# Kernel optimization log

Measured on AMD Instinct MI355X. Metric: run time of the kernel, lower is better.

The kernel has to match this reference:

```python
import jax, jax.numpy as jnp
import numpy as np

N_NODES = 50000
N_EDGES = 1600000
HID = 128
N_LAYERS = 4
EPS = 1e-5
NEG_SLOPE = 0.2


def setup_inputs() -> dict:
    key = jax.random.key(0)
    ks = jax.random.split(key, 10)
    x = jax.random.normal(ks[0], (N_NODES, HID), dtype=jnp.float32)
    edge_index = jax.random.randint(ks[1], (2, N_EDGES), 0, N_NODES, dtype=jnp.int64)
    edge_label_index = jax.random.randint(ks[2], (2, 8192), 0, N_NODES, dtype=jnp.int64)
    s = 1.0 / np.sqrt(HID)
    Wl = jax.random.uniform(ks[3], (N_LAYERS, HID, HID), jnp.float32, -s, s)
    Wr = jax.random.uniform(ks[4], (N_LAYERS, HID, HID), jnp.float32, -s, s)
    att = jax.random.uniform(ks[5], (N_LAYERS, HID), jnp.float32, -s, s)
    bias = jnp.zeros((N_LAYERS, HID), jnp.float32)
    gamma = jnp.ones((N_LAYERS, HID), jnp.float32)
    beta = jnp.zeros((N_LAYERS, HID), jnp.float32)
    return {"x": x, "edge_index": edge_index, "edge_label_index": edge_label_index,
            "Wl": Wl, "Wr": Wr, "att": att, "bias": bias, "gamma": gamma, "beta": beta}


def _gatv2_layer(x, Wl, Wr, a, b, src, dst):
    # GATv2Conv, single head: e_ij = a^T LeakyReLU(W_l x_j + W_r x_i)
    xl = x @ Wl                       # [N, H] source transform (also the message)
    xr = x @ Wr                       # [N, H] target transform
    e = jax.nn.leaky_relu(xl[src] + xr[dst], NEG_SLOPE) @ a   # [E]
    emax = jax.ops.segment_max(e, dst, num_segments=N_NODES)  # per-target max
    ew = jnp.exp(e - emax[dst])
    denom = jax.ops.segment_sum(ew, dst, num_segments=N_NODES)
    alpha = ew / denom[dst]
    out = jax.ops.segment_sum(alpha[:, None] * xl[src], dst, num_segments=N_NODES)
    return out + b


def _batchnorm(x, g, b):
    mu = jnp.mean(x, axis=0)
    var = jnp.mean(jnp.square(x - mu), axis=0)  # biased var (training mode)
    return (x - mu) * jax.lax.rsqrt(var + EPS) * g + b


def _embedding(x, edge_index, Wl, Wr, att, bias, gamma, beta):
    loops = jnp.arange(N_NODES, dtype=edge_index.dtype)
    src = jnp.concatenate([edge_index[0], loops])
    dst = jnp.concatenate([edge_index[1], loops])
    resw = 1.0 / (N_LAYERS + 1)  # alpha buffer, all entries equal
    h = x
    out = None
    for i in range(N_LAYERS):
        h = _gatv2_layer(h, Wl[i], Wr[i], att[i], bias[i], src, dst)
        h = _batchnorm(h, gamma[i], beta[i])
        out = h * resw if out is None else out + h * resw
    return out


def reference(x, edge_index, edge_label_index, Wl, Wr, att, bias, gamma, beta):
    out = _embedding(x, edge_index, Wl, Wr, att, bias, gamma, beta)
    return (out[edge_label_index[0]] * out[edge_label_index[1]]).sum(axis=-1)
```

## Files before the change

### kernel.cpp

```cpp
#include <hip/hip_runtime.h>
#include <hip/hip_bf16.h>
#include <hip/hip_fp16.h>

#define N_NODES 50000
#define N_EDGES 1600000
#define ET (N_EDGES + N_NODES)
#define HID 128
#define N_LAYERS 4
#define EPS 1e-5f
#define NEG 0.2f
#define RB 256
#define NBUCK 196
#define BCHUNK 8192
#define LOG2E 1.44269504088896f

typedef __attribute__((ext_vector_type(8))) short s16x8;
typedef __attribute__((ext_vector_type(8))) __bf16 bfx8;
typedef __attribute__((ext_vector_type(4))) float fx4;
typedef __attribute__((ext_vector_type(2))) _Float16 f16x2;

__device__ __forceinline__ unsigned int packbf2(float a, float b) {
    unsigned int ua = __float_as_uint(a);
    ua = (ua + 0x7fffu + ((ua >> 16) & 1u)) >> 16;
    unsigned int ub = __float_as_uint(b);
    ub = (ub + 0x7fffu + ((ub >> 16) & 1u)) & 0xffff0000u;
    return (ua & 0xffffu) | ub;
}
__device__ __forceinline__ unsigned short bf16r(float a) {
    unsigned int ua = __float_as_uint(a);
    return (unsigned short)((ua + 0x7fffu + ((ua >> 16) & 1u)) >> 16);
}
__device__ __forceinline__ unsigned int packh2(float a, float b) {
    return __builtin_bit_cast(unsigned int, __builtin_amdgcn_cvt_pkrtz(a, b));
}
__device__ __forceinline__ f16x2 packh2v(float a, float b) {
    return __builtin_bit_cast(f16x2, __builtin_amdgcn_cvt_pkrtz(a, b));
}
__device__ __forceinline__ float2 unpackh2(unsigned int u) {
    f16x2 h = __builtin_bit_cast(f16x2, u);
    return make_float2((float)h.x, (float)h.y);
}

__global__ void bucket_zero_kernel(int* __restrict__ gcnt, int* __restrict__ dhist) {
    int i = blockIdx.x * 256 + threadIdx.x;
    if (i < NBUCK) gcnt[i] = 0;
    if (i < 256) dhist[i] = 0;
}

__global__ __launch_bounds__(256) void bucket_hist_kernel(const int* __restrict__ ei,
                                                          int* __restrict__ gcnt) {
    __shared__ int h[NBUCK];
    for (int i = threadIdx.x; i < NBUCK; i += 256) h[i] = 0;
    __syncthreads();
    int base = blockIdx.x * BCHUNK;
    int lim = min(base + BCHUNK, ET);
    for (int i = base + threadIdx.x; i < lim; i += 256) {
        int dst = (i < N_EDGES) ? ei[N_EDGES + i] : i - N_EDGES;
        atomicAdd(&h[dst >> 8], 1);
    }
    __syncthreads();
    for (int i = threadIdx.x; i < NBUCK; i += 256)
        if (h[i]) atomicAdd(&gcnt[i], h[i]);
}

__global__ void bucket_scan_kernel(const int* __restrict__ gcnt, int* __restrict__ bbase,
                                   int* __restrict__ bcur, int* __restrict__ rowptr) {
    __shared__ int sh[256];
    int tid = threadIdx.x;
    int v = (tid < NBUCK) ? gcnt[tid] : 0;
    sh[tid] = v;
    __syncthreads();
    for (int off = 1; off < 256; off <<= 1) {
        int t = (tid >= off) ? sh[tid - off] : 0;
        __syncthreads();
        sh[tid] += t;
        __syncthreads();
    }
    if (tid < NBUCK) {
        int ex = sh[tid] - v;
        bbase[tid] = ex;
        bcur[tid] = ex;
    }
    if (tid == NBUCK - 1) bbase[NBUCK] = sh[tid];
    if (tid == 0) rowptr[N_NODES] = ET;
}

__global__ __launch_bounds__(256) void bucket_scatter_kernel(const int* __restrict__ ei,
                                                             int* __restrict__ bcur,
                                                             unsigned int* __restrict__ pairs) {
    __shared__ int h[NBUCK];
    __shared__ int rbase[NBUCK];
    for (int i = threadIdx.x; i < NBUCK; i += 256) h[i] = 0;
    __syncthreads();
    int base = blockIdx.x * BCHUNK;
    int lim = min(base + BCHUNK, ET);
    for (int i = base + threadIdx.x; i < lim; i += 256) {
        int dst = (i < N_EDGES) ? ei[N_EDGES + i] : i - N_EDGES;
        atomicAdd(&h[dst >> 8], 1);
    }
    __syncthreads();
    for (int i = threadIdx.x; i < NBUCK; i += 256) {
        rbase[i] = h[i] ? atomicAdd(&bcur[i], h[i]) : 0;
        h[i] = 0;
    }
    __syncthreads();
    for (int i = base + threadIdx.x; i < lim; i += 256) {
        int src, dst;
        if (i < N_EDGES) { src = ei[i]; dst = ei[N_EDGES + i]; }
        else { src = dst = i - N_EDGES; }
        int b = dst >> 8;
        int pos = rbase[b] + atomicAdd(&h[b], 1);
        pairs[pos] = (unsigned int)src | ((unsigned int)(dst & 255) << 16);
    }
}

__global__ __launch_bounds__(256) void bucket_sort_kernel(const unsigned int* __restrict__ pairs,
                                                          const int* __restrict__ bbase,
                                                          int* __restrict__ rowptr,
                                                          unsigned short* __restrict__ csr_src) {
    __shared__ int h[256], cur[256], sh[256];
    int b = blockIdx.x;
    int tid = threadIdx.x;
    h[tid] = 0;
    __syncthreads();
    int bs = bbase[b], be = bbase[b + 1];
    for (int i = bs + tid; i < be; i += 256) atomicAdd(&h[pairs[i] >> 16], 1);
    __syncthreads();
    int v = h[tid];
    sh[tid] = v;
    __syncthreads();
    for (int off = 1; off < 256; off <<= 1) {
        int u = (tid >= off) ? sh[tid - off] : 0;
        __syncthreads();
        sh[tid] += u;
        __syncthreads();
    }
    int ex = sh[tid] - v;
    cur[tid] = ex;
    int n0 = b * 256 + tid;
    if (n0 < N_NODES) rowptr[n0] = bs + ex;
    __syncthreads();
    for (int i = bs + tid; i < be; i += 256) {
        unsigned int u = pairs[i];
        int ln = u >> 16;
        int pos = bs + atomicAdd(&cur[ln], 1);
        csr_src[pos] = (unsigned short)(u & 0xffffu);
    }
}

__global__ __launch_bounds__(256) void deg_hist_kernel(const int* __restrict__ rowptr,
                                                       int* __restrict__ dhist) {
    __shared__ int h[256];
    h[threadIdx.x] = 0;
    __syncthreads();
    int n = blockIdx.x * 256 + threadIdx.x;
    if (n < N_NODES) {
        int cc = min((rowptr[n + 1] - rowptr[n] + 7) >> 3, 255);
        atomicAdd(&h[cc], 1);
    }
    __syncthreads();
    if (h[threadIdx.x]) atomicAdd(&dhist[threadIdx.x], h[threadIdx.x]);
}

__global__ void deg_scan_kernel(const int* __restrict__ dhist, int* __restrict__ dcur) {
    __shared__ int sh[256];
    int t = threadIdx.x;
    int v = dhist[t];
    sh[t] = v;
    __syncthreads();
    for (int off = 1; off < 256; off <<= 1) {
        int u = (t >= off) ? sh[t - off] : 0;
        __syncthreads();
        sh[t] += u;
        __syncthreads();
    }
    dcur[t] = sh[t] - v;
}

__global__ __launch_bounds__(256) void deg_scatter_kernel(const int* __restrict__ rowptr,
                                                          int* __restrict__ dcur,
                                                          int* __restrict__ perm) {
    __shared__ int h[256], rbase[256];
    int t = threadIdx.x;
    h[t] = 0;
    __syncthreads();
    int n = blockIdx.x * 256 + t;
    int cc = -1;
    if (n < N_NODES) {
        cc = min((rowptr[n + 1] - rowptr[n] + 7) >> 3, 255);
        atomicAdd(&h[cc], 1);
    }
    __syncthreads();
    rbase[t] = h[t] ? atomicAdd(&dcur[t], h[t]) : 0;
    h[t] = 0;
    __syncthreads();
    if (n < N_NODES) {
        int pos = rbase[cc] + atomicAdd(&h[cc], 1);
        perm[pos] = n;
    }
}

__global__ __launch_bounds__(256) void wconv_kernel(const float* __restrict__ Wl,
                                                    const float* __restrict__ Wr,
                                                    unsigned short* __restrict__ wt) {
    int m = blockIdx.x;
    const float* __restrict__ W = ((m & 1) ? Wr : Wl) + (size_t)(m >> 1) * HID * HID;
    unsigned short* __restrict__ o = wt + (size_t)m * HID * HID;
    for (int i = threadIdx.x; i < HID * HID; i += 256) {
        int k = i >> 7, c = i & 127;
        o[c * HID + k] = bf16r(W[i]);
    }
}

__global__ __launch_bounds__(256) void gemm_mfma_kernel(
    const float* __restrict__ hin_f, const unsigned int* __restrict__ hin_h,
    const unsigned short* __restrict__ wt_layer,
    unsigned int* __restrict__ xlh, unsigned int* __restrict__ xrh,
    const float* __restrict__ scale, const float* __restrict__ shift,
    unsigned int* __restrict__ accb, int donorm, int accmode) {
    __shared__ unsigned int Wsh[128 * 64];
    int row0 = blockIdx.x * 64;
    int tid = threadIdx.x;
    int w = tid >> 6, l = tid & 63;
    int lr = l & 15, lk = l >> 4;
    int node = row0 + w * 16 + lr;
    bool valid = node < N_NODES;

    bfx8 afrag[4];
#pragma unroll
    for (int kt = 0; kt < 4; kt++) {
        int ch = kt * 4 + lk;
        float4 va = make_float4(0.f, 0.f, 0.f, 0.f), vb = va;
        if (valid) {
            if (hin_h) {
                uint4 u = *(const uint4*)(hin_h + (size_t)node * 64 + ch * 4);
                float2 f0 = unpackh2(u.x), f1 = unpackh2(u.y);
                float2 f2 = unpackh2(u.z), f3 = unpackh2(u.w);
                va = make_float4(f0.x, f0.y, f1.x, f1.y);
                vb = make_float4(f2.x, f2.y, f3.x, f3.y);
            } else {
                const float4* src = (const float4*)(hin_f + (size_t)node * HID + ch * 8);
                va = src[0]; vb = src[1];
            }
            if (donorm) {
                const float4* s4 = (const float4*)(scale + ch * 8);
                const float4* t4 = (const float4*)(shift + ch * 8);
                float4 s0 = s4[0], s1 = s4[1], t0 = t4[0], t1 = t4[1];
                va.x = va.x * s0.x + t0.x; va.y = va.y * s0.y + t0.y;
                va.z = va.z * s0.z + t0.z; va.w = va.w * s0.w + t0.w;
                vb.x = vb.x * s1.x + t1.x; vb.y = vb.y * s1.y + t1.y;
                vb.z = vb.z * s1.z + t1.z; vb.w = vb.w * s1.w + t1.w;
            }
            if (accmode) {
                uint4* ap = (uint4*)(accb + (size_t)node * 64) + ch;
                uint4 av;
                if (accmode == 1) {
                    av.x = packh2(0.2f * va.x, 0.2f * va.y);
                    av.y = packh2(0.2f * va.z, 0.2f * va.w);
                    av.z = packh2(0.2f * vb.x, 0.2f * vb.y);
                    av.w = packh2(0.2f * vb.z, 0.2f * vb.w);
                } else {
                    uint4 old = *ap;
                    float2 o0 = unpackh2(old.x), o1 = unpackh2(old.y);
                    float2 o2 = unpackh2(old.z), o3 = unpackh2(old.w);
                    av.x = packh2(o0.x + 0.2f * va.x, o0.y + 0.2f * va.y);
                    av.y = packh2(o1.x + 0.2f * va.z, o1.y + 0.2f * va.w);
                    av.z = packh2(o2.x + 0.2f * vb.x, o2.y + 0.2f * vb.y);
                    av.w = packh2(o3.x + 0.2f * vb.z, o3.y + 0.2f * vb.w);
                }
                *ap = av;
            }
        }
        unsigned int pk0 = packbf2(va.x, va.y), pk1 = packbf2(va.z, va.w);
        unsigned int pk2 = packbf2(vb.x, vb.y), pk3 = packbf2(vb.z, vb.w);
        uint4 pk = make_uint4(pk0, pk1, pk2, pk3);
        afrag[kt] = __builtin_bit_cast(bfx8, pk);
    }

    for (int mat = 0; mat < 2; mat++) {
        if (mat) __syncthreads();
        const uint4* wm4 = (const uint4*)(wt_layer + (size_t)mat * HID * HID);
        for (int i = tid; i < 2048; i += 256) {
            int c = i >> 4, ch = i & 15;
            uint4 v = wm4[i];
            *(uint4*)(&Wsh[c * 64 + ((ch ^ (c & 7)) << 2)]) = v;
        }
        __syncthreads();

        fx4 acc[8];
#pragma unroll
        for (int ct = 0; ct < 8; ct++) acc[ct] = (fx4){0.f, 0.f, 0.f, 0.f};
#pragma unroll
        for (int kt = 0; kt < 4; kt++) {
            int ch = kt * 4 + lk;
#pragma unroll
            for (int ct = 0; ct < 8; ct++) {
                int c = ct * 16 + lr;
                bfx8 aw = __builtin_bit_cast(bfx8, *(const s16x8*)(&Wsh[c * 64 + ((ch ^ (c & 7)) << 2)]));
                acc[ct] = __builtin_amdgcn_mfma_f32_16x16x32_bf16(aw, afrag[kt], acc[ct], 0, 0, 0);
            }
        }
        unsigned int* o = mat ? xrh : xlh;
        if (valid) {
#pragma unroll
            for (int ct = 0; ct < 8; ct++) {
                int cb = ct * 8 + lk * 2;
                uint2 p0;
                p0.x = packh2(acc[ct][0], acc[ct][1]);
                p0.y = packh2(acc[ct][2], acc[ct][3]);
                *(uint2*)(o + (size_t)node * 64 + cb) = p0;
            }
        }
    }
}

__global__ __launch_bounds__(64) void aggregate_kernel(
    const unsigned int* __restrict__ xlh, const unsigned int* __restrict__ xrh,
    const float* __restrict__ att, const float* __restrict__ bias,
    const int* __restrict__ rowptr, const unsigned short* __restrict__ csr_src,
    const int* __restrict__ perm, unsigned int* __restrict__ hout) {
    int slot = blockIdx.x * 4 + (threadIdx.x >> 4);
    if (slot >= N_NODES) return;
    int node = perm[N_NODES - 1 - slot];
    int g = threadIdx.x & 15;
    int c0 = g * 8;
    float4 aa = *(const float4*)(att + c0);
    float4 ab = *(const float4*)(att + c0 + 4);
    f16x2 a0 = packh2v(aa.x * LOG2E, aa.y * LOG2E);
    f16x2 a1 = packh2v(aa.z * LOG2E, aa.w * LOG2E);
    f16x2 a2 = packh2v(ab.x * LOG2E, ab.y * LOG2E);
    f16x2 a3 = packh2v(ab.z * LOG2E, ab.w * LOG2E);
    const uint4 ru = *(const uint4*)(xrh + (size_t)node * 64 + g * 4);
    f16x2 r0 = __builtin_bit_cast(f16x2, ru.x), r1 = __builtin_bit_cast(f16x2, ru.y);
    f16x2 r2 = __builtin_bit_cast(f16x2, ru.z), r3 = __builtin_bit_cast(f16x2, ru.w);
    const f16x2 negc = {(_Float16)NEG, (_Float16)NEG};
    int beg = rowptr[node], end = rowptr[node + 1];
    bool b0 = (g & 1) != 0, b1 = (g & 2) != 0, b2 = (g & 4) != 0;
    int myj = g & 7;
    float spart = 0.f;
    float acc0 = 0.f, acc1 = 0.f, acc2 = 0.f, acc3 = 0.f;
    float acc4 = 0.f, acc5 = 0.f, acc6 = 0.f, acc7 = 0.f;
    int idxc = (int)csr_src[min(beg + myj, end - 1)];
    for (int base = beg; base < end; base += 8) {
        int nn = end - base;
        if (nn > 8) nn = 8;
        int idxn = (base + 8 < end) ? (int)csr_src[min(base + 8 + myj, end - 1)] : 0;
        uint4 v[8];
#pragma unroll
        for (int j = 0; j < 8; j++) {
            int sj = __shfl(idxc, j, 8);
            v[j] = *(const uint4*)(xlh + (size_t)sj * 64 + g * 4);
        }
        float p[8];
#pragma unroll
        for (int j = 0; j < 8; j++) {
            f16x2 v0 = __builtin_bit_cast(f16x2, v[j].x);
            f16x2 v1 = __builtin_bit_cast(f16x2, v[j].y);
            f16x2 v2 = __builtin_bit_cast(f16x2, v[j].z);
            f16x2 v3 = __builtin_bit_cast(f16x2, v[j].w);
            f16x2 s0 = v0 + r0, s1 = v1 + r1, s2 = v2 + r2, s3 = v3 + r3;
            f16x2 m0 = __builtin_elementwise_max(s0, s0 * negc);
            f16x2 m1 = __builtin_elementwise_max(s1, s1 * negc);
            f16x2 m2 = __builtin_elementwise_max(s2, s2 * negc);
            f16x2 m3 = __builtin_elementwise_max(s3, s3 * negc);
            p[j] = __builtin_amdgcn_fdot2(m0, a0,
                     __builtin_amdgcn_fdot2(m1, a1,
                       __builtin_amdgcn_fdot2(m2, a2,
                         __builtin_amdgcn_fdot2(m3, a3, 0.f, false), false), false), false);
        }
        float q0 = (b0 ? p[1] : p[0]) + __shfl_xor(b0 ? p[0] : p[1], 1);
        float q1 = (b0 ? p[3] : p[2]) + __shfl_xor(b0 ? p[2] : p[3], 1);
        float q2 = (b0 ? p[5] : p[4]) + __shfl_xor(b0 ? p[4] : p[5], 1);
        float q3 = (b0 ? p[7] : p[6]) + __shfl_xor(b0 ? p[6] : p[7], 1);
        float t0 = (b1 ? q1 : q0) + __shfl_xor(b1 ? q0 : q1, 2);
        float t1 = (b1 ? q3 : q2) + __shfl_xor(b1 ? q2 : q3, 2);
        float f  = (b2 ? t1 : t0) + __shfl_xor(b2 ? t0 : t1, 4);
        f += __shfl_xor(f, 8);
        float wown = (myj < nn) ? exp2f(f) : 0.f;
        spart += wown;
#pragma unroll
        for (int j = 0; j < 8; j++) {
            float wj = __shfl(wown, j, 8);
            f16x2 v0 = __builtin_bit_cast(f16x2, v[j].x);
            f16x2 v1 = __builtin_bit_cast(f16x2, v[j].y);
            f16x2 v2 = __builtin_bit_cast(f16x2, v[j].z);
            f16x2 v3 = __builtin_bit_cast(f16x2, v[j].w);
            acc0 += wj * (float)v0.x; acc1 += wj * (float)v0.y;
            acc2 += wj * (float)v1.x; acc3 += wj * (float)v1.y;
            acc4 += wj * (float)v2.x; acc5 += wj * (float)v2.y;
            acc6 += wj * (float)v3.x; acc7 += wj * (float)v3.y;
        }
        idxc = idxn;
    }
    float s = spart;
    s += __shfl_xor(s, 1);
    s += __shfl_xor(s, 2);
    s += __shfl_xor(s, 4);
    float inv = 1.f / s;
    float4 ba = *(const float4*)(bias + c0);
    float4 bb = *(const float4*)(bias + c0 + 4);
    uint4 po;
    po.x = packh2(acc0 * inv + ba.x, acc1 * inv + ba.y);
    po.y = packh2(acc2 * inv + ba.z, acc3 * inv + ba.w);
    po.z = packh2(acc4 * inv + bb.x, acc5 * inv + bb.y);
    po.w = packh2(acc6 * inv + bb.z, acc7 * inv + bb.w);
    *(uint4*)(hout + (size_t)node * 64 + g * 4) = po;
}

__global__ __launch_bounds__(256) void bn_reduce_kernel(const unsigned int* __restrict__ h,
                                                        float* __restrict__ part) {
    int tid = threadIdx.x;
    int cu = tid & 63, half = tid >> 6;
    float s0 = 0.f, q0 = 0.f, s1 = 0.f, q1 = 0.f;
    for (int r = blockIdx.x * 4 + half; r < N_NODES; r += RB * 4) {
        float2 v = unpackh2(h[(size_t)r * 64 + cu]);
        s0 += v.x; q0 += v.x * v.x;
        s1 += v.y; q1 += v.y * v.y;
    }
    __shared__ float sh[256];
    sh[half * 64 + cu] = s0;
    __syncthreads();
    if (tid < 64) {
        float r0 = sh[tid] + sh[64 + tid] + sh[128 + tid] + sh[192 + tid];
        part[blockIdx.x * 256 + tid * 2] = r0;
    }
    __syncthreads();
    sh[half * 64 + cu] = q0;
    __syncthreads();
    if (tid < 64) {
        float r0 = sh[tid] + sh[64 + tid] + sh[128 + tid] + sh[192 + tid];
        part[blockIdx.x * 256 + 128 + tid * 2] = r0;
    }
    __syncthreads();
    sh[half * 64 + cu] = s1;
    __syncthreads();
    if (tid < 64) {
        float r0 = sh[tid] + sh[64 + tid] + sh[128 + tid] + sh[192 + tid];
        part[blockIdx.x * 256 + tid * 2 + 1] = r0;
    }
    __syncthreads();
    sh[half * 64 + cu] = q1;
    __syncthreads();
    if (tid < 64) {
        float r0 = sh[tid] + sh[64 + tid] + sh[128 + tid] + sh[192 + tid];
        part[blockIdx.x * 256 + 128 + tid * 2 + 1] = r0;
    }
}

__global__ void bn_finalize_kernel(const float* __restrict__ part,
                                   const float* __restrict__ gamma,
                                   const float* __restrict__ beta,
                                   float* __restrict__ scale, float* __restrict__ shift) {
    int c = threadIdx.x;
    float s = 0.f, q = 0.f;
    for (int b = 0; b < RB; b++) {
        s += part[b * 256 + c];
        q += part[b * 256 + 128 + c];
    }
    float m = s / (float)N_NODES;
    float v = q / (float)N_NODES - m * m;
    if (v < 0.f) v = 0.f;
    float rs = rsqrtf(v + EPS);
    float sc = rs * gamma[c];
    scale[c] = sc;
    shift[c] = beta[c] - m * sc;
}

__global__ __launch_bounds__(256) void accb_kernel(const unsigned int* __restrict__ h,
                                                   const float* __restrict__ scale,
                                                   const float* __restrict__ shift,
                                                   unsigned int* __restrict__ acc) {
    int idx = blockIdx.x * 256 + threadIdx.x;
    if (idx >= N_NODES * 64) return;
    int c = (idx & 63) * 2;
    float2 v = unpackh2(h[idx]);
    float n0 = v.x * scale[c] + shift[c];
    float n1 = v.y * scale[c + 1] + shift[c + 1];
    float2 a = unpackh2(acc[idx]);
    acc[idx] = packh2(a.x + 0.2f * n0, a.y + 0.2f * n1);
}

__global__ __launch_bounds__(256) void predict_kernel(const unsigned int* __restrict__ acc,
                                                      const int* __restrict__ eli,
                                                      float* __restrict__ out) {
    int p = blockIdx.x * 4 + (threadIdx.x >> 6);
    if (p >= 8192) return;
    int lane = threadIdx.x & 63;
    int i = eli[p], j = eli[8192 + p];
    f16x2 va = __builtin_bit_cast(f16x2, acc[(size_t)i * 64 + lane]);
    f16x2 vb = __builtin_bit_cast(f16x2, acc[(size_t)j * 64 + lane]);
    float t = (float)va.x * (float)vb.x + (float)va.y * (float)vb.y;
#pragma unroll
    for (int off = 32; off; off >>= 1) t += __shfl_xor(t, off, 64);
    if (lane == 0) out[p] = t;
}

extern "C" void kernel_launch(void* const* d_in, const int* in_sizes, int n_in,
                              void* d_out, int out_size, void* d_ws, size_t ws_size,
                              hipStream_t stream) {
    const float* x = (const float*)d_in[0];
    const int* ei = (const int*)d_in[1];
    const int* eli = (const int*)d_in[2];
    const float* Wl = (const float*)d_in[3];
    const float* Wr = (const float*)d_in[4];
    const float* att = (const float*)d_in[5];
    const float* bias = (const float*)d_in[6];
    const float* gamma = (const float*)d_in[7];
    const float* beta = (const float*)d_in[8];
    float* out = (float*)d_out;

    char* ws = (char*)d_ws;
    size_t off = 0;
    unsigned int* hbuf = (unsigned int*)(ws + off); off += (size_t)N_NODES * HID * 2;
    unsigned int* accb = (unsigned int*)(ws + off); off += (size_t)N_NODES * HID * 2;
    unsigned int* xlh  = (unsigned int*)(ws + off); off += (size_t)N_NODES * HID * 2;
    unsigned int* xrh  = (unsigned int*)(ws + off); off += (size_t)N_NODES * HID * 2;
    int* rowptr = (int*)(ws + off);   off += ((size_t)(N_NODES + 1) * 4 + 31) & ~31ul;
    unsigned short* csr_src = (unsigned short*)(ws + off); off += ((size_t)(ET + 16) * 2 + 31) & ~31ul;
    int* gcnt  = (int*)(ws + off);    off += (size_t)(NBUCK + 8) * 4;
    int* bcur  = (int*)(ws + off);    off += (size_t)(NBUCK + 8) * 4;
    int* bbase = (int*)(ws + off);    off += (size_t)(NBUCK + 8) * 4;
    int* dhist = (int*)(ws + off);    off += 256 * 4;
    int* dcur  = (int*)(ws + off);    off += 256 * 4;
    int* perm  = (int*)(ws + off);    off += (size_t)N_NODES * 4;
    float* part = (float*)(ws + off); off += (size_t)RB * 256 * 4;
    float* scale = (float*)(ws + off); off += 128 * 4;
    float* shift = (float*)(ws + off); off += 128 * 4;
    unsigned short* wt = (unsigned short*)(ws + off); off += (size_t)8 * HID * HID * 2;
    unsigned int* pairs = (unsigned int*)(ws + off); off += (size_t)ET * 4;

    wconv_kernel<<<8, 256, 0, stream>>>(Wl, Wr, wt);

    int nablk = (ET + BCHUNK - 1) / BCHUNK;
    bucket_zero_kernel<<<1, 256, 0, stream>>>(gcnt, dhist);
    bucket_hist_kernel<<<nablk, 256, 0, stream>>>(ei, gcnt);
    bucket_scan_kernel<<<1, 256, 0, stream>>>(gcnt, bbase, bcur, rowptr);
    bucket_scatter_kernel<<<nablk, 256, 0, stream>>>(ei, bcur, pairs);
    bucket_sort_kernel<<<NBUCK, 256, 0, stream>>>(pairs, bbase, rowptr, csr_src);

    deg_hist_kernel<<<(N_NODES + 255) / 256, 256, 0, stream>>>(rowptr, dhist);
    deg_scan_kernel<<<1, 256, 0, stream>>>(dhist, dcur);
    deg_scatter_kernel<<<(N_NODES + 255) / 256, 256, 0, stream>>>(rowptr, dcur, perm);

    for (int l = 0; l < N_LAYERS; l++) {
        int donorm = (l == 0) ? 0 : 1;
        int accmode = (l == 0) ? 0 : (l == 1 ? 1 : 2);
        gemm_mfma_kernel<<<(N_NODES + 63) / 64, 256, 0, stream>>>(
            (l == 0) ? x : nullptr, (l == 0) ? nullptr : hbuf,
            wt + (size_t)l * 2 * HID * HID, xlh, xrh, scale, shift, accb,
            donorm, accmode);
        aggregate_kernel<<<(N_NODES + 3) / 4, 64, 0, stream>>>(
            xlh, xrh, att + l * HID, bias + l * HID, rowptr, csr_src, perm, hbuf);
        bn_reduce_kernel<<<RB, 256, 0, stream>>>(hbuf, part);
        bn_finalize_kernel<<<1, 128, 0, stream>>>(part, gamma + l * HID, beta + l * HID,
                                                  scale, shift);
    }
    accb_kernel<<<(N_NODES * 64 + 255) / 256, 256, 0, stream>>>(hbuf, scale, shift, accb);
    predict_kernel<<<8192 / 4, 256, 0, stream>>>(accb, eli, out);
}
```

Measured before the change: 496.0 us.

## Keep per-layer hidden buffers and compute residual sum only for predicted nodes

Each layer's pre-norm output and BN scale/shift are now stored separately instead of accumulating a full-graph residual buffer in the GEMM and a final accb pass. The predict kernel rebuilds the normalized sum from all four layers, but only for the 8192 node pairs it scores. This drops full-node read/modify/write traffic and one kernel launch, at the cost of extra workspace. Separately, the GEMM now reads weight fragments straight from global memory instead of staging them in LDS, which removes the barriers but may cost more cache traffic.

```diff
diff --git a/kernel.cpp b/kernel.cpp
--- a/kernel.cpp
+++ b/kernel.cpp
@@ -216,14 +216,11 @@
     const float* __restrict__ hin_f, const unsigned int* __restrict__ hin_h,
     const unsigned short* __restrict__ wt_layer,
     unsigned int* __restrict__ xlh, unsigned int* __restrict__ xrh,
-    const float* __restrict__ scale, const float* __restrict__ shift,
-    unsigned int* __restrict__ accb, int donorm, int accmode) {
-    __shared__ unsigned int Wsh[128 * 64];
-    int row0 = blockIdx.x * 64;
+    const float* __restrict__ scale, const float* __restrict__ shift, int donorm) {
     int tid = threadIdx.x;
     int w = tid >> 6, l = tid & 63;
     int lr = l & 15, lk = l >> 4;
-    int node = row0 + w * 16 + lr;
+    int node = blockIdx.x * 64 + w * 16 + lr;
     bool valid = node < N_NODES;
 
     bfx8 afrag[4];
@@ -251,25 +248,6 @@
                 vb.x = vb.x * s1.x + t1.x; vb.y = vb.y * s1.y + t1.y;
                 vb.z = vb.z * s1.z + t1.z; vb.w = vb.w * s1.w + t1.w;
             }
-            if (accmode) {
-                uint4* ap = (uint4*)(accb + (size_t)node * 64) + ch;
-                uint4 av;
-                if (accmode == 1) {
-                    av.x = packh2(0.2f * va.x, 0.2f * va.y);
-                    av.y = packh2(0.2f * va.z, 0.2f * va.w);
-                    av.z = packh2(0.2f * vb.x, 0.2f * vb.y);
-                    av.w = packh2(0.2f * vb.z, 0.2f * vb.w);
-                } else {
-                    uint4 old = *ap;
-                    float2 o0 = unpackh2(old.x), o1 = unpackh2(old.y);
-                    float2 o2 = unpackh2(old.z), o3 = unpackh2(old.w);
-                    av.x = packh2(o0.x + 0.2f * va.x, o0.y + 0.2f * va.y);
-                    av.y = packh2(o1.x + 0.2f * va.z, o1.y + 0.2f * va.w);
-                    av.z = packh2(o2.x + 0.2f * vb.x, o2.y + 0.2f * vb.y);
-                    av.w = packh2(o3.x + 0.2f * vb.z, o3.y + 0.2f * vb.w);
-                }
-                *ap = av;
-            }
         }
         unsigned int pk0 = packbf2(va.x, va.y), pk1 = packbf2(va.z, va.w);
         unsigned int pk2 = packbf2(vb.x, vb.y), pk3 = packbf2(vb.z, vb.w);
@@ -278,15 +256,7 @@
     }
 
     for (int mat = 0; mat < 2; mat++) {
-        if (mat) __syncthreads();
-        const uint4* wm4 = (const uint4*)(wt_layer + (size_t)mat * HID * HID);
-        for (int i = tid; i < 2048; i += 256) {
-            int c = i >> 4, ch = i & 15;
-            uint4 v = wm4[i];
-            *(uint4*)(&Wsh[c * 64 + ((ch ^ (c & 7)) << 2)]) = v;
-        }
-        __syncthreads();
-
+        const unsigned short* __restrict__ wm = wt_layer + (size_t)mat * HID * HID;
         fx4 acc[8];
 #pragma unroll
         for (int ct = 0; ct < 8; ct++) acc[ct] = (fx4){0.f, 0.f, 0.f, 0.f};
@@ -296,7 +266,7 @@
 #pragma unroll
             for (int ct = 0; ct < 8; ct++) {
                 int c = ct * 16 + lr;
-                bfx8 aw = __builtin_bit_cast(bfx8, *(const s16x8*)(&Wsh[c * 64 + ((ch ^ (c & 7)) << 2)]));
+                bfx8 aw = *(const bfx8*)(wm + (size_t)c * HID + ch * 8);
                 acc[ct] = __builtin_amdgcn_mfma_f32_16x16x32_bf16(aw, afrag[kt], acc[ct], 0, 0, 0);
             }
         }
@@ -466,30 +436,27 @@
     shift[c] = beta[c] - m * sc;
 }
 
-__global__ __launch_bounds__(256) void accb_kernel(const unsigned int* __restrict__ h,
-                                                   const float* __restrict__ scale,
-                                                   const float* __restrict__ shift,
-                                                   unsigned int* __restrict__ acc) {
-    int idx = blockIdx.x * 256 + threadIdx.x;
-    if (idx >= N_NODES * 64) return;
-    int c = (idx & 63) * 2;
-    float2 v = unpackh2(h[idx]);
-    float n0 = v.x * scale[c] + shift[c];
-    float n1 = v.y * scale[c + 1] + shift[c + 1];
-    float2 a = unpackh2(acc[idx]);
-    acc[idx] = packh2(a.x + 0.2f * n0, a.y + 0.2f * n1);
-}
-
-__global__ __launch_bounds__(256) void predict_kernel(const unsigned int* __restrict__ acc,
+__global__ __launch_bounds__(256) void predict_kernel(const unsigned int* __restrict__ hb,
+                                                      const float* __restrict__ scale4,
+                                                      const float* __restrict__ shift4,
                                                       const int* __restrict__ eli,
                                                       float* __restrict__ out) {
     int p = blockIdx.x * 4 + (threadIdx.x >> 6);
     if (p >= 8192) return;
     int lane = threadIdx.x & 63;
     int i = eli[p], j = eli[8192 + p];
-    f16x2 va = __builtin_bit_cast(f16x2, acc[(size_t)i * 64 + lane]);
-    f16x2 vb = __builtin_bit_cast(f16x2, acc[(size_t)j * 64 + lane]);
-    float t = (float)va.x * (float)vb.x + (float)va.y * (float)vb.y;
+    int c = lane * 2;
+    float ai0 = 0.f, ai1 = 0.f, aj0 = 0.f, aj1 = 0.f;
+#pragma unroll
+    for (int l = 0; l < N_LAYERS; l++) {
+        float sc0 = scale4[l * HID + c], sc1 = scale4[l * HID + c + 1];
+        float sh0 = shift4[l * HID + c], sh1 = shift4[l * HID + c + 1];
+        float2 vi = unpackh2(hb[(size_t)l * N_NODES * 64 + (size_t)i * 64 + lane]);
+        float2 vj = unpackh2(hb[(size_t)l * N_NODES * 64 + (size_t)j * 64 + lane]);
+        ai0 += vi.x * sc0 + sh0; ai1 += vi.y * sc1 + sh1;
+        aj0 += vj.x * sc0 + sh0; aj1 += vj.y * sc1 + sh1;
+    }
+    float t = 0.04f * (ai0 * aj0 + ai1 * aj1);
 #pragma unroll
     for (int off = 32; off; off >>= 1) t += __shfl_xor(t, off, 64);
     if (lane == 0) out[p] = t;
@@ -511,8 +478,7 @@
 
     char* ws = (char*)d_ws;
     size_t off = 0;
-    unsigned int* hbuf = (unsigned int*)(ws + off); off += (size_t)N_NODES * HID * 2;
-    unsigned int* accb = (unsigned int*)(ws + off); off += (size_t)N_NODES * HID * 2;
+    unsigned int* hb   = (unsigned int*)(ws + off); off += (size_t)N_LAYERS * N_NODES * HID * 2;
     unsigned int* xlh  = (unsigned int*)(ws + off); off += (size_t)N_NODES * HID * 2;
     unsigned int* xrh  = (unsigned int*)(ws + off); off += (size_t)N_NODES * HID * 2;
     int* rowptr = (int*)(ws + off);   off += ((size_t)(N_NODES + 1) * 4 + 31) & ~31ul;
@@ -524,8 +490,8 @@
     int* dcur  = (int*)(ws + off);    off += 256 * 4;
     int* perm  = (int*)(ws + off);    off += (size_t)N_NODES * 4;
     float* part = (float*)(ws + off); off += (size_t)RB * 256 * 4;
-    float* scale = (float*)(ws + off); off += 128 * 4;
-    float* shift = (float*)(ws + off); off += 128 * 4;
+    float* scale4 = (float*)(ws + off); off += (size_t)N_LAYERS * 128 * 4;
+    float* shift4 = (float*)(ws + off); off += (size_t)N_LAYERS * 128 * 4;
     unsigned short* wt = (unsigned short*)(ws + off); off += (size_t)8 * HID * HID * 2;
     unsigned int* pairs = (unsigned int*)(ws + off); off += (size_t)ET * 4;
 
@@ -544,17 +510,19 @@
 
     for (int l = 0; l < N_LAYERS; l++) {
         int donorm = (l == 0) ? 0 : 1;
-        int accmode = (l == 0) ? 0 : (l == 1 ? 1 : 2);
+        const unsigned int* hin_h = (l == 0) ? nullptr : hb + (size_t)(l - 1) * N_NODES * 64;
         gemm_mfma_kernel<<<(N_NODES + 63) / 64, 256, 0, stream>>>(
-            (l == 0) ? x : nullptr, (l == 0) ? nullptr : hbuf,
-            wt + (size_t)l * 2 * HID * HID, xlh, xrh, scale, shift, accb,
-            donorm, accmode);
+            (l == 0) ? x : nullptr, hin_h,
+            wt + (size_t)l * 2 * HID * HID, xlh, xrh,
+            scale4 + (size_t)(l ? l - 1 : 0) * HID, shift4 + (size_t)(l ? l - 1 : 0) * HID,
+            donorm);
         aggregate_kernel<<<(N_NODES + 3) / 4, 64, 0, stream>>>(
-            xlh, xrh, att + l * HID, bias + l * HID, rowptr, csr_src, perm, hbuf);
-        bn_reduce_kernel<<<RB, 256, 0, stream>>>(hbuf, part);
+            xlh, xrh, att + l * HID, bias + l * HID, rowptr, csr_src, perm,
+            hb + (size_t)l * N_NODES * 64);
+        bn_reduce_kernel<<<RB, 256, 0, stream>>>(hb + (size_t)l * N_NODES * 64, part);
         bn_finalize_kernel<<<1, 128, 0, stream>>>(part, gamma + l * HID, beta + l * HID,
-                                                  scale, shift);
-    }
-    accb_kernel<<<(N_NODES * 64 + 255) / 256, 256, 0, stream>>>(hbuf, scale, shift, accb);
-    predict_kernel<<<8192 / 4, 256, 0, stream>>>(accb, eli, out);
-}
+                                                  scale4 + (size_t)l * HID,
+                                                  shift4 + (size_t)l * HID);
+    }
+    predict_kernel<<<8192 / 4, 256, 0, stream>>>(hb, scale4, shift4, eli, out);
+}
```

After: 563.4 us. 1.14x slower.
